# Optimization experiments

Hardware: AMD Instinct MI355X
Metric: run time of the kernel (lower is better)

Reference implementation:

```python
import jax, jax.numpy as jnp
import numpy as np

# Fixed-point fake quantization: 8 total bits, 4 fractional bits (STE for grads)
FRAC_BITS = 4
TOTAL_BITS = 8
SCALE = 2.0 ** FRAC_BITS
QMIN = float(-(2 ** (TOTAL_BITS - 1)))
QMAX = float(2 ** (TOTAL_BITS - 1) - 1)


def fake_quant(x):
    q = jnp.clip(jnp.round(x * SCALE), QMIN, QMAX) / SCALE
    # straight-through estimator
    return x + jax.lax.stop_gradient(q - x)


def setup_inputs() -> dict:
    key = jax.random.key(0)
    ks = jax.random.split(key, 5)
    S, B, I, H = 2048, 64, 128, 256
    std = 1.0 / np.sqrt(H)  # pytorch LSTMCell default init range
    return {
        "x": jax.random.normal(ks[0], (S, B, I), jnp.float32),
        "weight_ih": jax.random.uniform(ks[1], (4 * H, I), jnp.float32, -std, std),
        "weight_hh": jax.random.uniform(ks[2], (4 * H, H), jnp.float32, -std, std),
        "bias_ih": jax.random.uniform(ks[3], (4 * H,), jnp.float32, -std, std),
        "bias_hh": jax.random.uniform(ks[4], (4 * H,), jnp.float32, -std, std),
    }


def reference(x, weight_ih, weight_hh, bias_ih, bias_hh):
    # x: [S, B, I] (batch_first=False). Gate order i, f, g, o (pytorch LSTMCell).
    B = x.shape[1]
    H = weight_hh.shape[1]
    # weight quantization is state-independent -> hoist out of the scan
    wi = fake_quant(weight_ih)  # [4H, I]
    wh = fake_quant(weight_hh)  # [4H, H]
    bi = fake_quant(bias_ih)
    bh = fake_quant(bias_hh)

    def step(carry, x_t):
        h, c = carry
        hq = fake_quant(h)
        cq = fake_quant(c)
        gates = x_t @ wi.T + bi + hq @ wh.T + bh  # [B, 4H]
        i_g, f_g, g_g, o_g = jnp.split(gates, 4, axis=1)
        i = jax.nn.sigmoid(i_g)
        f = jax.nn.sigmoid(f_g)
        g = jnp.tanh(g_g)
        o = jax.nn.sigmoid(o_g)
        c1 = f * cq + i * g
        h1 = o * jnp.tanh(c1)
        return (h1, c1), h1

    zeros = jnp.zeros((B, H), x.dtype)
    (h_n, c_n), outputs = jax.lax.scan(step, (zeros, zeros), x)
    return outputs, h_n, c_n
```

## Files before the change

kernel.cpp:

```cpp
#include <hip/hip_runtime.h>
#include <math.h>

#define S_LEN 2048
#define BATCH 64
#define IN_D  128
#define HID   256
#define G4    1024

#if defined(__has_builtin)
# if __has_builtin(__builtin_amdgcn_sdot4)
#  define USE_SDOT4 1
# endif
#endif

__device__ __forceinline__ int dot4i8(int a, int b, int c) {
#ifdef USE_SDOT4
    return __builtin_amdgcn_sdot4(a, b, c, false);
#else
    int r = c;
    r += ((a << 24) >> 24) * ((b << 24) >> 24);
    r += ((a << 16) >> 24) * ((b << 16) >> 24);
    r += ((a <<  8) >> 24) * ((b <<  8) >> 24);
    r += ( a        >> 24) * ( b        >> 24);
    return r;
#endif
}

__device__ __forceinline__ float fq4(float x) {
    return fminf(fmaxf(rintf(x * 16.0f), -128.0f), 127.0f) * 0.0625f;
}

__device__ __forceinline__ float exp_vsl(float x) {
    const float xc = fminf(fmaxf(x, -88.3762626647949f), 88.3762626647950f);
    const float fx = floorf(fmaf(xc, 1.44269504088896341f, 0.5f));
    float r = fmaf(-fx, 0.693359375f, xc);
    r = fmaf(fx, 2.12194440e-4f, r);
    const float z = __fmul_rn(r, r);
    float y = fmaf(r, 1.9875691500e-4f, 1.3981999507e-3f);
    y = fmaf(y, r, 8.3334519073e-3f);
    y = fmaf(y, r, 4.1665795894e-2f);
    y = fmaf(y, r, 1.6666665459e-1f);
    y = fmaf(y, r, 5.0000001201e-1f);
    y = fmaf(y, z, r);
    y = __fadd_rn(y, 1.0f);
    const int n = (int)fx;
    const float sc = __int_as_float((n + 127) << 23);
    return __fmul_rn(y, sc);
}

__device__ __forceinline__ float tanh_vsl(float x) {
    const float xc = fminf(fmaxf(x, -9.0f), 9.0f);
    const float x2 = __fmul_rn(xc, xc);
    float p = -2.76076847742355e-16f;
    p = fmaf(p, x2, 2.00018790482477e-13f);
    p = fmaf(p, x2, -8.60467152213735e-11f);
    p = fmaf(p, x2, 5.12229709037114e-08f);
    p = fmaf(p, x2, 1.48572235717979e-05f);
    p = fmaf(p, x2, 6.37261928875436e-04f);
    p = fmaf(p, x2, 4.89352455891786e-03f);
    p = __fmul_rn(p, xc);
    float q = 1.19825839466702e-06f;
    q = fmaf(q, x2, 1.18534705686654e-04f);
    q = fmaf(q, x2, 2.26843463243900e-03f);
    q = fmaf(q, x2, 4.89352518554385e-03f);
    return __fdiv_rn(p, q);
}

__device__ __forceinline__ float sig_vsl(float x) {
    const float ef = exp_vsl(-x);
    return __fdiv_rn(1.0f, __fadd_rn(1.0f, ef));
}

__global__ void qlstm_prep(const float* __restrict__ wih, const float* __restrict__ whh,
                           const float* __restrict__ bih, const float* __restrict__ bhh,
                           float* __restrict__ wiq, int* __restrict__ whqT,
                           float* __restrict__ biq, float* __restrict__ bhq,
                           float* __restrict__ c_state, int* __restrict__ hq_state) {
    const int idx = blockIdx.x * 256 + threadIdx.x;
    if (idx < G4 * IN_D) wiq[idx] = fq4(wih[idx]);
    if (idx < (HID / 4) * G4) {
        const int d = idx >> 10;
        const int j = idx & 1023;
        int pack = 0;
#pragma unroll
        for (int c = 0; c < 4; ++c) {
            const int k = d * 4 + c;
            float q = fminf(fmaxf(rintf(whh[j * HID + k] * 16.0f), -128.0f), 127.0f);
            int qi = (int)q;
            pack |= (qi & 0xff) << (8 * c);
        }
        whqT[idx] = pack;
    }
    if (idx < G4) { biq[idx] = fq4(bih[idx]); bhq[idx] = fq4(bhh[idx]); }
    if (idx < BATCH * HID) c_state[idx] = 0.0f;
    if (idx < BATCH * (HID / 4)) hq_state[idx] = 0;
}

#define GPAD 132
__global__ __launch_bounds__(256, 1) void qlstm_gx(
    const float* __restrict__ X, const float* __restrict__ Wq,
    const float* __restrict__ biq, float* __restrict__ Gx, int Mc) {
    __shared__ float Xs[IN_D][GPAD];
    __shared__ float Ws[IN_D][GPAD];
    const int t  = threadIdx.x;
    const int m0 = blockIdx.x * 128;
    const int n0 = blockIdx.y * 128;

#pragma unroll
    for (int i = 0; i < 16; ++i) {
        const int flat = i * 256 + t;
        const int m  = flat >> 5;
        const int k4 = flat & 31;
        float4 v = make_float4(0.f, 0.f, 0.f, 0.f);
        if (m0 + m < Mc) v = *(const float4*)(X + (size_t)(m0 + m) * IN_D + k4 * 4);
        Xs[k4 * 4 + 0][m] = v.x; Xs[k4 * 4 + 1][m] = v.y;
        Xs[k4 * 4 + 2][m] = v.z; Xs[k4 * 4 + 3][m] = v.w;
        float4 w = *(const float4*)(Wq + (size_t)(n0 + m) * IN_D + k4 * 4);
        Ws[k4 * 4 + 0][m] = w.x; Ws[k4 * 4 + 1][m] = w.y;
        Ws[k4 * 4 + 2][m] = w.z; Ws[k4 * 4 + 3][m] = w.w;
    }
    __syncthreads();

    const int tx = t & 15, ty = t >> 4;
    float acc[8][8];
#pragma unroll
    for (int i = 0; i < 8; ++i)
#pragma unroll
        for (int j = 0; j < 8; ++j) acc[i][j] = 0.0f;

#pragma unroll 4
    for (int k = 0; k < IN_D; ++k) {
        float4 a0 = *(const float4*)&Xs[k][ty * 8];
        float4 a1 = *(const float4*)&Xs[k][ty * 8 + 4];
        float4 b0 = *(const float4*)&Ws[k][tx * 8];
        float4 b1 = *(const float4*)&Ws[k][tx * 8 + 4];
        const float a[8]  = {a0.x, a0.y, a0.z, a0.w, a1.x, a1.y, a1.z, a1.w};
        const float bb[8] = {b0.x, b0.y, b0.z, b0.w, b1.x, b1.y, b1.z, b1.w};
#pragma unroll
        for (int i = 0; i < 8; ++i)
#pragma unroll
            for (int j = 0; j < 8; ++j)
                acc[i][j] = __fadd_rn(acc[i][j], __fmul_rn(a[i], bb[j]));
    }

    float4 bv0 = *(const float4*)(biq + n0 + tx * 8);
    float4 bv1 = *(const float4*)(biq + n0 + tx * 8 + 4);
    const float bb[8] = {bv0.x, bv0.y, bv0.z, bv0.w, bv1.x, bv1.y, bv1.z, bv1.w};
#pragma unroll
    for (int i = 0; i < 8; ++i) {
        const int m = m0 + ty * 8 + i;
        if (m < Mc) {
            float o[8];
#pragma unroll
            for (int j = 0; j < 8; ++j) o[j] = __fadd_rn(acc[i][j], bb[j]);
            *(float4*)(Gx + (size_t)m * G4 + n0 + tx * 8)     = make_float4(o[0], o[1], o[2], o[3]);
            *(float4*)(Gx + (size_t)m * G4 + n0 + tx * 8 + 4) = make_float4(o[4], o[5], o[6], o[7]);
        }
    }
}

__global__ __launch_bounds__(1024, 4) void qlstm_scan(
    const float* __restrict__ Gx, const int* __restrict__ whqT,
    const float* __restrict__ bhq,
    float* __restrict__ out, float* __restrict__ c_state, int* __restrict__ hq_state,
    float* __restrict__ hn, float* __restrict__ cn, int s0, int CHc) {
    const int b = blockIdx.x;
    const int t = threadIdx.x;

    __shared__ __align__(16) int hq[2][64];
    __shared__ float gl[G4];

    int w[64];
#pragma unroll
    for (int d = 0; d < 64; ++d) w[d] = whqT[d * G4 + t];
#pragma unroll
    for (int d = 0; d < 64; ++d) asm volatile("" : "+v"(w[d]));

    const float bh = bhq[t];

    float creg = 0.0f;
    if (t < HID) creg = c_state[b * HID + t];
    if (t < 64)  hq[0][t] = hq_state[b * 64 + t];
    __syncthreads();

    float gx = Gx[(size_t)b * G4 + t];

    for (int sl = 0; sl < CHc; ++sl) {
        const int p = sl & 1;
        float nx = 0.0f;
        if (sl + 1 < CHc) nx = Gx[(size_t)((sl + 1) * BATCH + b) * G4 + t];

        int ca0 = 0, ca1 = 0, ca2 = 0, ca3 = 0;
#pragma unroll
        for (int d = 0; d < 4; ++d) {
            const int4 h0 = ((const int4*)hq[p])[d];
            const int4 h1 = ((const int4*)hq[p])[4 + d];
            const int4 h2 = ((const int4*)hq[p])[8 + d];
            const int4 h3 = ((const int4*)hq[p])[12 + d];
            ca0 = dot4i8(w[d * 4 + 0], h0.x, ca0);
            ca0 = dot4i8(w[d * 4 + 1], h0.y, ca0);
            ca0 = dot4i8(w[d * 4 + 2], h0.z, ca0);
            ca0 = dot4i8(w[d * 4 + 3], h0.w, ca0);
            ca1 = dot4i8(w[16 + d * 4 + 0], h1.x, ca1);
            ca1 = dot4i8(w[16 + d * 4 + 1], h1.y, ca1);
            ca1 = dot4i8(w[16 + d * 4 + 2], h1.z, ca1);
            ca1 = dot4i8(w[16 + d * 4 + 3], h1.w, ca1);
            ca2 = dot4i8(w[32 + d * 4 + 0], h2.x, ca2);
            ca2 = dot4i8(w[32 + d * 4 + 1], h2.y, ca2);
            ca2 = dot4i8(w[32 + d * 4 + 2], h2.z, ca2);
            ca2 = dot4i8(w[32 + d * 4 + 3], h2.w, ca2);
            ca3 = dot4i8(w[48 + d * 4 + 0], h3.x, ca3);
            ca3 = dot4i8(w[48 + d * 4 + 1], h3.y, ca3);
            ca3 = dot4i8(w[48 + d * 4 + 2], h3.z, ca3);
            ca3 = dot4i8(w[48 + d * 4 + 3], h3.w, ca3);
        }
        const int acc = (ca0 + ca1) + (ca2 + ca3);

        const float hh = (float)acc * 0.00390625f;
        const float gate = __fadd_rn(__fadd_rn(gx, hh), bh);

        float tv;
        if (t < 512)       tv = sig_vsl(gate);
        else if (t < 768)  tv = tanh_vsl(gate);
        else               tv = sig_vsl(gate);
        gl[t] = tv;
        __syncthreads();

        if (t < HID) {
            const float fv = gl[t + 256];
            const float gv = gl[t + 512];
            const float ov = gl[t + 768];
            const float cq = fminf(fmaxf(rintf(__fmul_rn(creg, 16.0f)), -128.0f), 127.0f) * 0.0625f;
            const float c1 = fmaf(fv, cq, __fmul_rn(tv, gv));
            const float h1 = __fmul_rn(ov, tanh_vsl(c1));
            creg = c1;
            out[(size_t)((s0 + sl) * BATCH + b) * HID + t] = h1;
            const int hb = (int)fminf(fmaxf(rintf(__fmul_rn(h1, 16.0f)), -128.0f), 127.0f);
            ((signed char*)hq[p ^ 1])[t] = (signed char)hb;
            if (s0 + sl == S_LEN - 1) {
                hn[b * HID + t] = h1;
                cn[b * HID + t] = c1;
            }
        }
        __syncthreads();
        gx = nx;
    }

    if (t < 64)  hq_state[b * 64 + t] = hq[CHc & 1][t];
    if (t < HID) c_state[b * HID + t] = creg;
}

extern "C" void kernel_launch(void* const* d_in, const int* in_sizes, int n_in,
                              void* d_out, int out_size, void* d_ws, size_t ws_size,
                              hipStream_t stream) {
    (void)in_sizes; (void)n_in; (void)out_size;
    const float* x   = (const float*)d_in[0];
    const float* wih = (const float*)d_in[1];
    const float* whh = (const float*)d_in[2];
    const float* bih = (const float*)d_in[3];
    const float* bhh = (const float*)d_in[4];

    float* out = (float*)d_out;
    float* hn  = out + (size_t)S_LEN * BATCH * HID;
    float* cn  = hn + (size_t)BATCH * HID;

    char* ws = (char*)d_ws;
    const size_t off_wiq  = 0;
    const size_t off_whqT = off_wiq  + 524288;
    const size_t off_biq  = off_whqT + 262144;
    const size_t off_bhq  = off_biq  + 4096;
    const size_t off_c    = off_bhq  + 4096;
    const size_t off_hq   = off_c    + 65536;
    const size_t off_gx   = off_hq   + 16384;

    float* wiq     = (float*)(ws + off_wiq);
    int*   whqT    = (int*)  (ws + off_whqT);
    float* biq     = (float*)(ws + off_biq);
    float* bhq     = (float*)(ws + off_bhq);
    float* c_state = (float*)(ws + off_c);
    int*   hq_st   = (int*)  (ws + off_hq);
    float* gx      = (float*)(ws + off_gx);

    const size_t per_step = (size_t)BATCH * G4 * 4;
    size_t avail = (ws_size > off_gx) ? (ws_size - off_gx) : 0;
    int CH = (int)(avail / per_step);
    if (CH > S_LEN) CH = S_LEN;
    if (CH < 1) CH = 1;

    qlstm_prep<<<512, 256, 0, stream>>>(wih, whh, bih, bhh, wiq, whqT, biq, bhq, c_state, hq_st);

    for (int s0 = 0; s0 < S_LEN; s0 += CH) {
        const int CHc = (S_LEN - s0 < CH) ? (S_LEN - s0) : CH;
        const int Mc  = CHc * BATCH;
        dim3 grid((Mc + 127) / 128, G4 / 128);
        qlstm_gx<<<grid, 256, 0, stream>>>(x + (size_t)s0 * BATCH * IN_D, wiq, biq, gx, Mc);
        qlstm_scan<<<64, 1024, 0, stream>>>(gx, whqT, bhq, out, c_state, hq_st, hn, cn, s0, CHc);
    }
}
```

Before: 3.111 ms.

## Overlap next chunk's input GEMM with recurrent scan in a fused kernel

The scan and input-projection GEMM are fused into one launch. 64 blocks run the recurrence for the current chunk while 192 extra blocks compute the Gx projection for the next chunk into a double buffer. The recurrent int8 weights are no longer held in 64 registers per thread. They are repacked so each step reloads them from global/L2 as int4 vectors, which removes register pressure but adds memory traffic on every timestep. Chunk size is capped at 512 so the GEMM work can be pipelined, at the cost of more launches and contention between scan and GEMM blocks.

```diff
diff --git a/kernel.cpp b/kernel.cpp
--- a/kernel.cpp
+++ b/kernel.cpp
@@ -73,7 +73,7 @@
 
 __global__ void qlstm_prep(const float* __restrict__ wih, const float* __restrict__ whh,
                            const float* __restrict__ bih, const float* __restrict__ bhh,
-                           float* __restrict__ wiq, int* __restrict__ whqT,
+                           float* __restrict__ wiq, int* __restrict__ whq4,
                            float* __restrict__ biq, float* __restrict__ bhq,
                            float* __restrict__ c_state, int* __restrict__ hq_state) {
     const int idx = blockIdx.x * 256 + threadIdx.x;
@@ -89,7 +89,7 @@
             int qi = (int)q;
             pack |= (qi & 0xff) << (8 * c);
         }
-        whqT[idx] = pack;
+        whq4[(d >> 2) * 4096 + j * 4 + (d & 3)] = pack;
     }
     if (idx < G4) { biq[idx] = fq4(bih[idx]); bhq[idx] = fq4(bhh[idx]); }
     if (idx < BATCH * HID) c_state[idx] = 0.0f;
@@ -159,95 +159,168 @@
     }
 }
 
-__global__ __launch_bounds__(1024, 4) void qlstm_scan(
-    const float* __restrict__ Gx, const int* __restrict__ whqT,
-    const float* __restrict__ bhq,
+__global__ __launch_bounds__(1024) void qlstm_fused(
+    const float* __restrict__ Gx_rd, float* __restrict__ Gx_wr,
+    const float* __restrict__ Xn, const float* __restrict__ Wq,
+    const float* __restrict__ biq, int Mc_next,
+    const int* __restrict__ whq4, const float* __restrict__ bhq,
     float* __restrict__ out, float* __restrict__ c_state, int* __restrict__ hq_state,
     float* __restrict__ hn, float* __restrict__ cn, int s0, int CHc) {
-    const int b = blockIdx.x;
     const int t = threadIdx.x;
 
+    __shared__ float Xs[IN_D][GPAD];
+    __shared__ float Ws[IN_D][GPAD];
     __shared__ __align__(16) int hq[2][64];
     __shared__ float gl[G4];
 
-    int w[64];
-#pragma unroll
-    for (int d = 0; d < 64; ++d) w[d] = whqT[d * G4 + t];
-#pragma unroll
-    for (int d = 0; d < 64; ++d) asm volatile("" : "+v"(w[d]));
-
-    const float bh = bhq[t];
-
-    float creg = 0.0f;
-    if (t < HID) creg = c_state[b * HID + t];
-    if (t < 64)  hq[0][t] = hq_state[b * 64 + t];
-    __syncthreads();
-
-    float gx = Gx[(size_t)b * G4 + t];
-
-    for (int sl = 0; sl < CHc; ++sl) {
-        const int p = sl & 1;
-        float nx = 0.0f;
-        if (sl + 1 < CHc) nx = Gx[(size_t)((sl + 1) * BATCH + b) * G4 + t];
-
-        int ca0 = 0, ca1 = 0, ca2 = 0, ca3 = 0;
-#pragma unroll
-        for (int d = 0; d < 4; ++d) {
-            const int4 h0 = ((const int4*)hq[p])[d];
-            const int4 h1 = ((const int4*)hq[p])[4 + d];
-            const int4 h2 = ((const int4*)hq[p])[8 + d];
-            const int4 h3 = ((const int4*)hq[p])[12 + d];
-            ca0 = dot4i8(w[d * 4 + 0], h0.x, ca0);
-            ca0 = dot4i8(w[d * 4 + 1], h0.y, ca0);
-            ca0 = dot4i8(w[d * 4 + 2], h0.z, ca0);
-            ca0 = dot4i8(w[d * 4 + 3], h0.w, ca0);
-            ca1 = dot4i8(w[16 + d * 4 + 0], h1.x, ca1);
-            ca1 = dot4i8(w[16 + d * 4 + 1], h1.y, ca1);
-            ca1 = dot4i8(w[16 + d * 4 + 2], h1.z, ca1);
-            ca1 = dot4i8(w[16 + d * 4 + 3], h1.w, ca1);
-            ca2 = dot4i8(w[32 + d * 4 + 0], h2.x, ca2);
-            ca2 = dot4i8(w[32 + d * 4 + 1], h2.y, ca2);
-            ca2 = dot4i8(w[32 + d * 4 + 2], h2.z, ca2);
-            ca2 = dot4i8(w[32 + d * 4 + 3], h2.w, ca2);
-            ca3 = dot4i8(w[48 + d * 4 + 0], h3.x, ca3);
-            ca3 = dot4i8(w[48 + d * 4 + 1], h3.y, ca3);
-            ca3 = dot4i8(w[48 + d * 4 + 2], h3.z, ca3);
-            ca3 = dot4i8(w[48 + d * 4 + 3], h3.w, ca3);
+    if (blockIdx.x < 64) {
+        const int b = blockIdx.x;
+
+        const float bh = bhq[t];
+        float creg = 0.0f;
+        if (t < HID) creg = c_state[b * HID + t];
+        if (t < 64)  hq[0][t] = hq_state[b * 64 + t];
+        __syncthreads();
+
+        float gx = Gx_rd[(size_t)b * G4 + t];
+
+        for (int sl = 0; sl < CHc; ++sl) {
+            const int p = sl & 1;
+            float nx = 0.0f;
+            if (sl + 1 < CHc) nx = Gx_rd[(size_t)((sl + 1) * BATCH + b) * G4 + t];
+
+            const int4* __restrict__ wq = (const int4*)whq4;
+            const int4* __restrict__ hv4 = (const int4*)hq[p];
+            int ca0 = 0, ca1 = 0, ca2 = 0, ca3 = 0;
+#pragma unroll
+            for (int j = 0; j < 4; ++j) {
+                const int4 wv = wq[j * 1024 + t];
+                const int4 hv = hv4[j];
+                ca0 = dot4i8(wv.x, hv.x, ca0);
+                ca0 = dot4i8(wv.y, hv.y, ca0);
+                ca0 = dot4i8(wv.z, hv.z, ca0);
+                ca0 = dot4i8(wv.w, hv.w, ca0);
+            }
+#pragma unroll
+            for (int j = 4; j < 8; ++j) {
+                const int4 wv = wq[j * 1024 + t];
+                const int4 hv = hv4[j];
+                ca1 = dot4i8(wv.x, hv.x, ca1);
+                ca1 = dot4i8(wv.y, hv.y, ca1);
+                ca1 = dot4i8(wv.z, hv.z, ca1);
+                ca1 = dot4i8(wv.w, hv.w, ca1);
+            }
+#pragma unroll
+            for (int j = 8; j < 12; ++j) {
+                const int4 wv = wq[j * 1024 + t];
+                const int4 hv = hv4[j];
+                ca2 = dot4i8(wv.x, hv.x, ca2);
+                ca2 = dot4i8(wv.y, hv.y, ca2);
+                ca2 = dot4i8(wv.z, hv.z, ca2);
+                ca2 = dot4i8(wv.w, hv.w, ca2);
+            }
+#pragma unroll
+            for (int j = 12; j < 16; ++j) {
+                const int4 wv = wq[j * 1024 + t];
+                const int4 hv = hv4[j];
+                ca3 = dot4i8(wv.x, hv.x, ca3);
+                ca3 = dot4i8(wv.y, hv.y, ca3);
+                ca3 = dot4i8(wv.z, hv.z, ca3);
+                ca3 = dot4i8(wv.w, hv.w, ca3);
+            }
+            const int acc = (ca0 + ca1) + (ca2 + ca3);
+
+            const float hh = (float)acc * 0.00390625f;
+            const float gate = __fadd_rn(__fadd_rn(gx, hh), bh);
+
+            float tv;
+            if (t < 512)       tv = sig_vsl(gate);
+            else if (t < 768)  tv = tanh_vsl(gate);
+            else               tv = sig_vsl(gate);
+            gl[t] = tv;
+            __syncthreads();
+
+            if (t < HID) {
+                const float fv = gl[t + 256];
+                const float gv = gl[t + 512];
+                const float ov = gl[t + 768];
+                const float cq = fminf(fmaxf(rintf(__fmul_rn(creg, 16.0f)), -128.0f), 127.0f) * 0.0625f;
+                const float c1 = fmaf(fv, cq, __fmul_rn(tv, gv));
+                const float h1 = __fmul_rn(ov, tanh_vsl(c1));
+                creg = c1;
+                out[(size_t)((s0 + sl) * BATCH + b) * HID + t] = h1;
+                const int hb = (int)fminf(fmaxf(rintf(__fmul_rn(h1, 16.0f)), -128.0f), 127.0f);
+                ((signed char*)hq[p ^ 1])[t] = (signed char)hb;
+                if (s0 + sl == S_LEN - 1) {
+                    hn[b * HID + t] = h1;
+                    cn[b * HID + t] = c1;
+                }
+            }
+            __syncthreads();
+            gx = nx;
         }
-        const int acc = (ca0 + ca1) + (ca2 + ca3);
-
-        const float hh = (float)acc * 0.00390625f;
-        const float gate = __fadd_rn(__fadd_rn(gx, hh), bh);
-
-        float tv;
-        if (t < 512)       tv = sig_vsl(gate);
-        else if (t < 768)  tv = tanh_vsl(gate);
-        else               tv = sig_vsl(gate);
-        gl[t] = tv;
-        __syncthreads();
-
-        if (t < HID) {
-            const float fv = gl[t + 256];
-            const float gv = gl[t + 512];
-            const float ov = gl[t + 768];
-            const float cq = fminf(fmaxf(rintf(__fmul_rn(creg, 16.0f)), -128.0f), 127.0f) * 0.0625f;
-            const float c1 = fmaf(fv, cq, __fmul_rn(tv, gv));
-            const float h1 = __fmul_rn(ov, tanh_vsl(c1));
-            creg = c1;
-            out[(size_t)((s0 + sl) * BATCH + b) * HID + t] = h1;
-            const int hb = (int)fminf(fmaxf(rintf(__fmul_rn(h1, 16.0f)), -128.0f), 127.0f);
-            ((signed char*)hq[p ^ 1])[t] = (signed char)hb;
-            if (s0 + sl == S_LEN - 1) {
-                hn[b * HID + t] = h1;
-                cn[b * HID + t] = c1;
-            }
+
+        if (t < 64)  hq_state[b * 64 + t] = hq[CHc & 1][t];
+        if (t < HID) c_state[b * HID + t] = creg;
+    } else if (Mc_next > 0) {
+        const int wid = blockIdx.x - 64;
+        const int tiles_m = (Mc_next + 127) / 128;
+        const int total = tiles_m * 8;
+        const int tx = t & 31, ty = t >> 5;
+
+        for (int tile = wid; tile < total; tile += 192) {
+            const int m0 = (tile >> 3) * 128;
+            const int n0 = (tile & 7) * 128;
+
+#pragma unroll
+            for (int i = 0; i < 4; ++i) {
+                const int flat = i * 1024 + t;
+                const int m  = flat >> 5;
+                const int k4 = flat & 31;
+                float4 v = make_float4(0.f, 0.f, 0.f, 0.f);
+                if (m0 + m < Mc_next) v = *(const float4*)(Xn + (size_t)(m0 + m) * IN_D + k4 * 4);
+                Xs[k4 * 4 + 0][m] = v.x; Xs[k4 * 4 + 1][m] = v.y;
+                Xs[k4 * 4 + 2][m] = v.z; Xs[k4 * 4 + 3][m] = v.w;
+                float4 w = *(const float4*)(Wq + (size_t)(n0 + m) * IN_D + k4 * 4);
+                Ws[k4 * 4 + 0][m] = w.x; Ws[k4 * 4 + 1][m] = w.y;
+                Ws[k4 * 4 + 2][m] = w.z; Ws[k4 * 4 + 3][m] = w.w;
+            }
+            __syncthreads();
+
+            float acc[4][4];
+#pragma unroll
+            for (int i = 0; i < 4; ++i)
+#pragma unroll
+                for (int j = 0; j < 4; ++j) acc[i][j] = 0.0f;
+
+#pragma unroll 4
+            for (int k = 0; k < IN_D; ++k) {
+                float4 av = *(const float4*)&Xs[k][ty * 4];
+                float4 bv = *(const float4*)&Ws[k][tx * 4];
+                const float a[4]  = {av.x, av.y, av.z, av.w};
+                const float bb[4] = {bv.x, bv.y, bv.z, bv.w};
+#pragma unroll
+                for (int i = 0; i < 4; ++i)
+#pragma unroll
+                    for (int j = 0; j < 4; ++j)
+                        acc[i][j] = __fadd_rn(acc[i][j], __fmul_rn(a[i], bb[j]));
+            }
+
+            float4 bv = *(const float4*)(biq + n0 + tx * 4);
+            const float bb[4] = {bv.x, bv.y, bv.z, bv.w};
+#pragma unroll
+            for (int i = 0; i < 4; ++i) {
+                const int m = m0 + ty * 4 + i;
+                if (m < Mc_next) {
+                    float o[4];
+#pragma unroll
+                    for (int j = 0; j < 4; ++j) o[j] = __fadd_rn(acc[i][j], bb[j]);
+                    *(float4*)(Gx_wr + (size_t)m * G4 + n0 + tx * 4) = make_float4(o[0], o[1], o[2], o[3]);
+                }
+            }
+            __syncthreads();
         }
-        __syncthreads();
-        gx = nx;
-    }
-
-    if (t < 64)  hq_state[b * 64 + t] = hq[CHc & 1][t];
-    if (t < HID) c_state[b * HID + t] = creg;
+    }
 }
 
 extern "C" void kernel_launch(void* const* d_in, const int* in_sizes, int n_in,
@@ -266,34 +339,45 @@
 
     char* ws = (char*)d_ws;
     const size_t off_wiq  = 0;
-    const size_t off_whqT = off_wiq  + 524288;
-    const size_t off_biq  = off_whqT + 262144;
+    const size_t off_biq  = off_wiq  + 524288;
     const size_t off_bhq  = off_biq  + 4096;
     const size_t off_c    = off_bhq  + 4096;
     const size_t off_hq   = off_c    + 65536;
-    const size_t off_gx   = off_hq   + 16384;
+    const size_t off_whq4 = off_hq   + 16384;
+    const size_t off_gx   = off_whq4 + 262144;
 
     float* wiq     = (float*)(ws + off_wiq);
-    int*   whqT    = (int*)  (ws + off_whqT);
     float* biq     = (float*)(ws + off_biq);
     float* bhq     = (float*)(ws + off_bhq);
     float* c_state = (float*)(ws + off_c);
     int*   hq_st   = (int*)  (ws + off_hq);
-    float* gx      = (float*)(ws + off_gx);
+    int*   whq4    = (int*)  (ws + off_whq4);
+    float* gxbase  = (float*)(ws + off_gx);
 
     const size_t per_step = (size_t)BATCH * G4 * 4;
     size_t avail = (ws_size > off_gx) ? (ws_size - off_gx) : 0;
-    int CH = (int)(avail / per_step);
-    if (CH > S_LEN) CH = S_LEN;
+    int CH = (int)(avail / (2 * per_step));
+    if (CH > 512) CH = 512;
     if (CH < 1) CH = 1;
-
-    qlstm_prep<<<512, 256, 0, stream>>>(wih, whh, bih, bhh, wiq, whqT, biq, bhq, c_state, hq_st);
-
-    for (int s0 = 0; s0 < S_LEN; s0 += CH) {
+    float* gxb[2] = { gxbase, gxbase + (size_t)CH * BATCH * G4 };
+
+    qlstm_prep<<<512, 256, 0, stream>>>(wih, whh, bih, bhh, wiq, whq4, biq, bhq, c_state, hq_st);
+
+    const int CHc0 = (S_LEN < CH) ? S_LEN : CH;
+    const int Mc0  = CHc0 * BATCH;
+    {
+        dim3 grid((Mc0 + 127) / 128, G4 / 128);
+        qlstm_gx<<<grid, 256, 0, stream>>>(x, wiq, biq, gxb[0], Mc0);
+    }
+
+    int k = 0;
+    for (int s0 = 0; s0 < S_LEN; s0 += CH, ++k) {
         const int CHc = (S_LEN - s0 < CH) ? (S_LEN - s0) : CH;
-        const int Mc  = CHc * BATCH;
-        dim3 grid((Mc + 127) / 128, G4 / 128);
-        qlstm_gx<<<grid, 256, 0, stream>>>(x + (size_t)s0 * BATCH * IN_D, wiq, biq, gx, Mc);
-        qlstm_scan<<<64, 1024, 0, stream>>>(gx, whqT, bhq, out, c_state, hq_st, hn, cn, s0, CHc);
-    }
-}
+        const int ns0 = s0 + CHc;
+        const int Mc_next = (ns0 < S_LEN) ? (((S_LEN - ns0 < CH) ? (S_LEN - ns0) : CH) * BATCH) : 0;
+        qlstm_fused<<<256, 1024, 0, stream>>>(
+            gxb[k & 1], gxb[(k + 1) & 1],
+            x + (size_t)ns0 * BATCH * IN_D, wiq, biq, Mc_next,
+            whq4, bhq, out, c_state, hq_st, hn, cn, s0, CHc);
+    }
+}
```

New measurement: 2.688 ms. 13.6% less time.
